# Optimization experiments

Hardware: AMD Instinct MI355X
Metric: run time of the kernel (lower is better)

## Reference

```python
import jax, jax.numpy as jnp
import numpy as np

L, D, F, V = 24, 1024, 4096, 50277  # n_layer, n_embd, ffn hidden (4*D), vocab
RESCALE = 6


def _ln(x, w, b, eps=1e-5):
    m = jnp.mean(x, axis=-1, keepdims=True)
    v = jnp.mean(jnp.square(x - m), axis=-1, keepdims=True)
    return (x - m) * jax.lax.rsqrt(v + eps) * w + b


def setup_inputs() -> dict:
    key = jax.random.key(0)
    ks = iter(jax.random.split(key, 64))

    def nrm(shape, s=0.02):
        return jax.random.normal(next(ks), shape, jnp.float32) * s

    def uni(shape):
        return jax.random.uniform(next(ks), shape, jnp.float32)

    state = jnp.zeros((L, 5, D), jnp.float32).at[:, 4, :].set(-1e30)  # pp init
    return {
        "token_embd": jax.random.normal(next(ks), (D,), jnp.float32),
        "state": state,
        "emb_ln_w": jnp.ones((D,), jnp.float32),
        "emb_ln_b": jnp.zeros((D,), jnp.float32),
        "ln1_w": jnp.ones((L, D), jnp.float32),
        "ln1_b": jnp.zeros((L, D), jnp.float32),
        "ln2_w": jnp.ones((L, D), jnp.float32),
        "ln2_b": jnp.zeros((L, D), jnp.float32),
        "att_tmk": uni((L, D)),
        "att_tmv": uni((L, D)),
        "att_tmr": uni((L, D)),
        "att_tf": nrm((L, D), 0.5),
        "att_td": -jnp.exp(nrm((L, D), 0.5)),  # time_decay = -exp(w) at load
        "att_kw": nrm((L, D, D)),
        "att_vw": nrm((L, D, D)),
        "att_rw": nrm((L, D, D)),
        "att_ow": nrm((L, D, D)),
        "ffn_tmk": uni((L, D)),
        "ffn_tmr": uni((L, D)),
        "ffn_kw": nrm((L, F, D)),
        "ffn_vw": nrm((L, D, F)),
        "ffn_rw": nrm((L, D, D)),
        "out_ln_w": jnp.ones((D,), jnp.float32),
        "out_ln_b": jnp.zeros((D,), jnp.float32),
        "head_w": nrm((V, D)),
    }


def reference(token_embd, state, emb_ln_w, emb_ln_b, ln1_w, ln1_b, ln2_w, ln2_b,
              att_tmk, att_tmv, att_tmr, att_tf, att_td, att_kw, att_vw, att_rw,
              att_ow, ffn_tmk, ffn_tmr, ffn_kw, ffn_vw, ffn_rw,
              out_ln_w, out_ln_b, head_w):
    x0 = _ln(token_embd, emb_ln_w, emb_ln_b)  # encoder

    def layer(x, inputs):
        (i, st, l1w, l1b, l2w, l2b, tmk, tmv, tmr, tf, td,
         kw, vw, rw, ow, ftmk, ftmr, fkw, fvw, frw) = inputs
        # ---- time mixing ----
        xn = _ln(x, l1w, l1b)
        s_att, aa, bb, pp = st[1], st[2], st[3], st[4]
        xk = xn * tmk + s_att * (1 - tmk)
        xv = xn * tmv + s_att * (1 - tmv)
        xr = xn * tmr + s_att * (1 - tmr)
        r = jax.nn.sigmoid(rw @ xr)
        kk = kw @ xk
        vv = vw @ xv
        ww = tf + kk
        p = jnp.maximum(pp, ww)
        e1 = jnp.exp(pp - p)
        e2 = jnp.exp(ww - p)
        a = e1 * aa + e2 * vv
        b = e1 * bb + e2
        ww2 = pp + td
        p2 = jnp.maximum(ww2, kk)
        f1 = jnp.exp(ww2 - p2)
        f2 = jnp.exp(kk - p2)
        new_aa = f1 * aa + f2 * vv
        new_bb = f1 * bb + f2
        x = x + ow @ (r * (a / b))
        # ---- channel mixing ----
        xn2 = _ln(x, l2w, l2b)
        s_ffn = st[0]
        xk2 = xn2 * ftmk + s_ffn * (1 - ftmk)
        xr2 = xn2 * ftmr + s_ffn * (1 - ftmr)
        r2 = jax.nn.sigmoid(frw @ xr2)
        k2 = jnp.square(jax.nn.relu(fkw @ xk2))
        x = x + r2 * (fvw @ k2)
        # rescale every RESCALE layers
        x = jnp.where((i + 1) % RESCALE == 0, x * 0.5, x)
        new_st = jnp.stack([xn2, xn, new_aa, new_bb, p2])
        return x, new_st

    idx = jnp.arange(L)
    x, new_state = jax.lax.scan(
        layer, x0,
        (idx, state, ln1_w, ln1_b, ln2_w, ln2_b, att_tmk, att_tmv, att_tmr,
         att_tf, att_td, att_kw, att_vw, att_rw, att_ow, ffn_tmk, ffn_tmr,
         ffn_kw, ffn_vw, ffn_rw))
    logits = head_w @ _ln(x, out_ln_w, out_ln_b)  # decoder
    return logits, new_state
```

## Files before the change

kernel.cpp:

```cpp
#include <hip/hip_runtime.h>

#define DD 1024
#define FF 4096
#define LL 24
#define VV 50277

typedef float v4f __attribute__((ext_vector_type(4)));


__device__ __forceinline__ float wave_sum(float v) {
#pragma unroll
    for (int o = 32; o > 0; o >>= 1) v += __shfl_xor(v, o, 64);
    return v;
}

__device__ __forceinline__ v4f ln_fast(v4f x, const float* __restrict__ w,
                                       const float* __restrict__ b,
                                       float* scr, int t) {
    float s1 = x[0] + x[1] + x[2] + x[3];
    float s2 = x[0]*x[0] + x[1]*x[1] + x[2]*x[2] + x[3]*x[3];
    s1 = wave_sum(s1); s2 = wave_sum(s2);
    int wv = t >> 6;
    __syncthreads();
    if ((t & 63) == 0) { scr[wv] = s1; scr[4 + wv] = s2; }
    __syncthreads();
    float S1 = scr[0] + scr[1] + scr[2] + scr[3];
    float S2 = scr[4] + scr[5] + scr[6] + scr[7];
    float m = S1 * (1.0f / 1024.0f);
    float var = S2 * (1.0f / 1024.0f) - m * m;
    float rs = rsqrtf(var + 1e-5f);
    v4f w4 = ((const v4f*)w)[t], b4 = ((const v4f*)b)[t];
    return (x - m) * rs * w4 + b4;
}

__device__ __forceinline__ v4f mixv(v4f n, v4f s, v4f m) { return n * m + s * (1.0f - m); }

__device__ __forceinline__ float dotv(v4f a, v4f x) {
    return fmaf(a[0], x[0], fmaf(a[1], x[1], fmaf(a[2], x[2], a[3] * x[3])));
}

struct Row { v4f a, b, c, d; };

__device__ __forceinline__ void row_load(Row& r, const float* p, int lane) {
    const v4f* q = (const v4f*)p;
    r.a = q[lane]; r.b = q[lane + 64]; r.c = q[lane + 128]; r.d = q[lane + 192];
}
__device__ __forceinline__ void row_pin(Row& r) {
    asm volatile("" : "+v"(r.a), "+v"(r.b), "+v"(r.c), "+v"(r.d));
}
__device__ __forceinline__ float row_dot(const Row& r, const v4f* v, int lane) {
    return dotv(r.a, v[lane]) + dotv(r.b, v[lane + 64]) +
           dotv(r.c, v[lane + 128]) + dotv(r.d, v[lane + 192]);
}


__global__ __launch_bounds__(256) void k1_timemix(
    const float* __restrict__ xin, const float* __restrict__ st,
    const float* __restrict__ enc_w, const float* __restrict__ enc_b,
    const float* __restrict__ l1w, const float* __restrict__ l1b,
    const float* __restrict__ tmk, const float* __restrict__ tmv,
    const float* __restrict__ tmr,
    const float* __restrict__ kw, const float* __restrict__ vw,
    const float* __restrict__ rw,
    float* __restrict__ kk, float* __restrict__ vv, float* __restrict__ rr,
    float* __restrict__ x0out, float* __restrict__ st_out) {
    __shared__ __align__(16) v4f s_k[256], s_v[256], s_r[256];
    __shared__ float scr[8];
    const int t = threadIdx.x, lane = t & 63, w = t >> 6, b = blockIdx.x;

    const int ridx = 4 * b + w, m = ridx >> 10, row = ridx & 1023;
    Row W;
    row_load(W, (m == 0 ? kw : m == 1 ? vw : rw) + (size_t)row * DD, lane);
    row_pin(W);

    v4f xv = ((const v4f*)xin)[t];
    if (enc_w) xv = ln_fast(xv, enc_w, enc_b, scr, t);
    if (x0out && b == 0) ((v4f*)x0out)[t] = xv;
    v4f n = ln_fast(xv, l1w, l1b, scr, t);
    if (b == 0) ((v4f*)(st_out + DD))[t] = n;
    {
        v4f sa = ((const v4f*)(st + DD))[t];
        s_k[t] = mixv(n, sa, ((const v4f*)tmk)[t]);
        s_v[t] = mixv(n, sa, ((const v4f*)tmv)[t]);
        s_r[t] = mixv(n, sa, ((const v4f*)tmr)[t]);
    }
    __syncthreads();

    const v4f* vec = (m == 0) ? s_k : (m == 1) ? s_v : s_r;
    float acc = wave_sum(row_dot(W, vec, lane));
    if (lane == 0) {
        if (m == 0)      kk[row] = acc;
        else if (m == 1) vv[row] = acc;
        else             rr[row] = 1.0f / (1.0f + expf(-acc));
    }
}


__global__ __launch_bounds__(256) void k2_wkv_out(
    const float* __restrict__ st, const float* __restrict__ tf,
    const float* __restrict__ td,
    const float* __restrict__ kk, const float* __restrict__ vv,
    const float* __restrict__ rr, const float* __restrict__ ow,
    float* __restrict__ x, float* __restrict__ st_out) {
    __shared__ __align__(16) v4f rab[256];
    const int t = threadIdx.x, lane = t & 63, w = t >> 6, b = blockIdx.x;

    const int row = 4 * b + w;
    Row W;
    row_load(W, ow + (size_t)row * DD, lane);
    row_pin(W);

    {
        v4f kx = ((const v4f*)kk)[t];
        v4f vx = ((const v4f*)vv)[t];
        v4f rx = ((const v4f*)rr)[t];
        v4f aa = ((const v4f*)(st + 2 * DD))[t];
        v4f bb = ((const v4f*)(st + 3 * DD))[t];
        v4f pp = ((const v4f*)(st + 4 * DD))[t];
        v4f tf4 = ((const v4f*)tf)[t];
        v4f td4 = ((const v4f*)td)[t];
        v4f rb, naa, nbb, np2;
#pragma unroll
        for (int c = 0; c < 4; ++c) {
            float kc = kx[c], vc = vx[c];
            float wwc = tf4[c] + kc;
            float p = fmaxf(pp[c], wwc);
            float e1 = expf(pp[c] - p), e2 = expf(wwc - p);
            rb[c] = rx[c] * ((e1 * aa[c] + e2 * vc) / (e1 * bb[c] + e2));
            float ww2 = pp[c] + td4[c];
            float p2 = fmaxf(ww2, kc);
            float f1 = expf(ww2 - p2), f2 = expf(kc - p2);
            naa[c] = f1 * aa[c] + f2 * vc;
            nbb[c] = f1 * bb[c] + f2;
            np2[c] = p2;
        }
        rab[t] = rb;
        if (b == 0) {
            ((v4f*)(st_out + 2 * DD))[t] = naa;
            ((v4f*)(st_out + 3 * DD))[t] = nbb;
            ((v4f*)(st_out + 4 * DD))[t] = np2;
        }
    }
    __syncthreads();

    float acc = wave_sum(row_dot(W, &rab[0], lane));
    if (lane == 0) x[row] += acc;
}


__global__ __launch_bounds__(256) void k3_ffn_kr(
    const float* __restrict__ x, const float* __restrict__ st,
    const float* __restrict__ l2w, const float* __restrict__ l2b,
    const float* __restrict__ ftmk, const float* __restrict__ ftmr,
    const float* __restrict__ fkw, const float* __restrict__ frw,
    float* __restrict__ k2, float* __restrict__ r2, float* __restrict__ st_out) {
    __shared__ __align__(16) v4f s_k[256], s_r[256];
    __shared__ float scr[8];
    const int t = threadIdx.x, lane = t & 63, w = t >> 6, b = blockIdx.x;

    const int ridx = 4 * b + w;
    Row W;
    row_load(W, (ridx < FF ? fkw + (size_t)ridx * DD
                           : frw + (size_t)(ridx - FF) * DD), lane);
    row_pin(W);

    v4f xv = ((const v4f*)x)[t];
    v4f n = ln_fast(xv, l2w, l2b, scr, t);
    if (b == 0) ((v4f*)st_out)[t] = n;
    {
        v4f sf = ((const v4f*)st)[t];
        s_k[t] = mixv(n, sf, ((const v4f*)ftmk)[t]);
        s_r[t] = mixv(n, sf, ((const v4f*)ftmr)[t]);
    }
    __syncthreads();

    const v4f* vec = (ridx < FF) ? s_k : s_r;
    float acc = wave_sum(row_dot(W, vec, lane));
    if (lane == 0) {
        if (ridx < FF) { float rl = fmaxf(acc, 0.f); k2[ridx] = rl * rl; }
        else           r2[ridx - FF] = 1.0f / (1.0f + expf(-acc));
    }
}


__global__ __launch_bounds__(256) void k4_ffn_v(
    const float* __restrict__ fvw, const float* __restrict__ k2,
    const float* __restrict__ r2, float* __restrict__ x, float scale) {
    __shared__ __align__(16) v4f k2s[1024];
    const int t = threadIdx.x, lane = t & 63, w = t >> 6, b = blockIdx.x;
    const int row = 4 * b + w;
    const v4f* W4 = (const v4f*)(fvw + (size_t)row * FF);

    v4f h0 = W4[lane],       h1 = W4[lane + 64],  h2 = W4[lane + 128], h3 = W4[lane + 192];
    v4f h4 = W4[lane + 256], h5 = W4[lane + 320], h6 = W4[lane + 384], h7 = W4[lane + 448];
    asm volatile("" : "+v"(h0), "+v"(h1), "+v"(h2), "+v"(h3),
                      "+v"(h4), "+v"(h5), "+v"(h6), "+v"(h7));

#pragma unroll
    for (int j = 0; j < 4; ++j)
        k2s[t + 256 * j] = ((const v4f*)k2)[t + 256 * j];
    __syncthreads();

    float acc = dotv(h0, k2s[lane])       + dotv(h1, k2s[lane + 64]) +
                dotv(h2, k2s[lane + 128]) + dotv(h3, k2s[lane + 192]) +
                dotv(h4, k2s[lane + 256]) + dotv(h5, k2s[lane + 320]) +
                dotv(h6, k2s[lane + 384]) + dotv(h7, k2s[lane + 448]);
#pragma unroll
    for (int j = 8; j < 16; ++j) {
        v4f a = W4[lane + 64 * j];
        acc += dotv(a, k2s[lane + 64 * j]);
    }
    acc = wave_sum(acc);
    if (lane == 0) x[row] = (x[row] + r2[row] * acc) * scale;
}


__global__ __launch_bounds__(256) void k_head(const float* __restrict__ head_w,
                                              const float* __restrict__ x,
                                              const float* __restrict__ olw,
                                              const float* __restrict__ olb,
                                              float* __restrict__ logits) {
    __shared__ __align__(16) v4f xs[256];
    __shared__ float scr[8];
    const int t = threadIdx.x, lane = t & 63, w = t >> 6;
    const int row = blockIdx.x * 4 + w;
    Row W;
    if (row < VV) { row_load(W, head_w + (size_t)row * DD, lane); row_pin(W); }

    v4f xv = ((const v4f*)x)[t];
    v4f nx = ln_fast(xv, olw, olb, scr, t);
    xs[t] = nx;
    __syncthreads();
    if (row < VV) {
        float acc = wave_sum(row_dot(W, &xs[0], lane));
        if (lane == 0) logits[row] = acc;
    }
}


extern "C" void kernel_launch(void* const* d_in, const int* in_sizes, int n_in,
                              void* d_out, int out_size, void* d_ws, size_t ws_size,
                              hipStream_t stream) {
    const float* token_embd = (const float*)d_in[0];
    const float* state      = (const float*)d_in[1];
    const float* emb_ln_w   = (const float*)d_in[2];
    const float* emb_ln_b   = (const float*)d_in[3];
    const float* ln1_w      = (const float*)d_in[4];
    const float* ln1_b      = (const float*)d_in[5];
    const float* ln2_w      = (const float*)d_in[6];
    const float* ln2_b      = (const float*)d_in[7];
    const float* att_tmk    = (const float*)d_in[8];
    const float* att_tmv    = (const float*)d_in[9];
    const float* att_tmr    = (const float*)d_in[10];
    const float* att_tf     = (const float*)d_in[11];
    const float* att_td     = (const float*)d_in[12];
    const float* att_kw     = (const float*)d_in[13];
    const float* att_vw     = (const float*)d_in[14];
    const float* att_rw     = (const float*)d_in[15];
    const float* att_ow     = (const float*)d_in[16];
    const float* ffn_tmk    = (const float*)d_in[17];
    const float* ffn_tmr    = (const float*)d_in[18];
    const float* ffn_kw     = (const float*)d_in[19];
    const float* ffn_vw     = (const float*)d_in[20];
    const float* ffn_rw     = (const float*)d_in[21];
    const float* out_ln_w   = (const float*)d_in[22];
    const float* out_ln_b   = (const float*)d_in[23];
    const float* head_w     = (const float*)d_in[24];

    float* logits = (float*)d_out;
    float* st_out_base = (float*)d_out + VV;

    float* ws  = (float*)d_ws;
    float* x   = ws;
    float* kk  = ws + 1024;
    float* vv  = ws + 2048;
    float* rr  = ws + 3072;
    float* k2b = ws + 4096;
    float* r2b = ws + 8192;

    for (int i = 0; i < LL; ++i) {
        const float* st = state + (size_t)i * 5 * DD;
        float* sto = st_out_base + (size_t)i * 5 * DD;

        k1_timemix<<<768, 256, 0, stream>>>(
            (i == 0) ? token_embd : x, st,
            (i == 0) ? emb_ln_w : nullptr, (i == 0) ? emb_ln_b : nullptr,
            ln1_w + i * DD, ln1_b + i * DD,
            att_tmk + i * DD, att_tmv + i * DD, att_tmr + i * DD,
            att_kw + (size_t)i * DD * DD, att_vw + (size_t)i * DD * DD,
            att_rw + (size_t)i * DD * DD,
            kk, vv, rr, (i == 0) ? x : nullptr, sto);

        k2_wkv_out<<<256, 256, 0, stream>>>(
            st, att_tf + i * DD, att_td + i * DD, kk, vv, rr,
            att_ow + (size_t)i * DD * DD, x, sto);

        k3_ffn_kr<<<1280, 256, 0, stream>>>(
            x, st, ln2_w + i * DD, ln2_b + i * DD,
            ffn_tmk + i * DD, ffn_tmr + i * DD,
            ffn_kw + (size_t)i * FF * DD, ffn_rw + (size_t)i * DD * DD,
            k2b, r2b, sto);

        float scale = ((i + 1) % 6 == 0) ? 0.5f : 1.0f;
        k4_ffn_v<<<256, 256, 0, stream>>>(
            ffn_vw + (size_t)i * DD * FF, k2b, r2b, x, scale);
    }

    k_head<<<(VV + 3) / 4, 256, 0, stream>>>(head_w, x, out_ln_w, out_ln_b, logits);
}
```

Baseline: 595.8 us.

## Fuse WKV into time-mix kernel and split output GEMVs across more blocks

The time-mix kernel now launches 768-thread blocks, each computing the k, v and r rows for the same 4 channels. That lets it evaluate the WKV recurrence and state update in-block and write r*wkv directly. The separate WKV pass is removed, and the att_ow and ffn_vw GEMVs are re-split so each block handles one output row across 4 waves (1024 blocks instead of 256). The aim is to raise parallelism and memory-level concurrency on bandwidth-bound matvecs and to drop one intermediate round-trip. In exchange it adds extra block-level reductions, and the LayerNorm in k1 runs with 12 waves, 8 of them idle.

```diff
diff --git a/kernel.cpp b/kernel.cpp
--- a/kernel.cpp
+++ b/kernel.cpp
@@ -14,22 +14,25 @@
     return v;
 }
 
-__device__ __forceinline__ v4f ln_fast(v4f x, const float* __restrict__ w,
-                                       const float* __restrict__ b,
-                                       float* scr, int t) {
-    float s1 = x[0] + x[1] + x[2] + x[3];
-    float s2 = x[0]*x[0] + x[1]*x[1] + x[2]*x[2] + x[3]*x[3];
+template <int NW>
+__device__ __forceinline__ v4f ln_gen(v4f x, const float* __restrict__ w,
+                                      const float* __restrict__ b,
+                                      float* scr, int t, bool act) {
+    float s1 = act ? (x[0] + x[1] + x[2] + x[3]) : 0.f;
+    float s2 = act ? (x[0]*x[0] + x[1]*x[1] + x[2]*x[2] + x[3]*x[3]) : 0.f;
     s1 = wave_sum(s1); s2 = wave_sum(s2);
     int wv = t >> 6;
     __syncthreads();
-    if ((t & 63) == 0) { scr[wv] = s1; scr[4 + wv] = s2; }
-    __syncthreads();
-    float S1 = scr[0] + scr[1] + scr[2] + scr[3];
-    float S2 = scr[4] + scr[5] + scr[6] + scr[7];
+    if ((t & 63) == 0) { scr[wv] = s1; scr[NW + wv] = s2; }
+    __syncthreads();
+    float S1 = 0.f, S2 = 0.f;
+#pragma unroll
+    for (int i = 0; i < NW; ++i) { S1 += scr[i]; S2 += scr[NW + i]; }
     float m = S1 * (1.0f / 1024.0f);
     float var = S2 * (1.0f / 1024.0f) - m * m;
     float rs = rsqrtf(var + 1e-5f);
-    v4f w4 = ((const v4f*)w)[t], b4 = ((const v4f*)b)[t];
+    v4f w4 = act ? ((const v4f*)w)[t] : (v4f){0.f, 0.f, 0.f, 0.f};
+    v4f b4 = act ? ((const v4f*)b)[t] : (v4f){0.f, 0.f, 0.f, 0.f};
     return (x - m) * rs * w4 + b4;
 }
 
@@ -54,97 +57,83 @@
 }
 
 
-__global__ __launch_bounds__(256) void k1_timemix(
+__global__ __launch_bounds__(768) void k1_timemix(
     const float* __restrict__ xin, const float* __restrict__ st,
     const float* __restrict__ enc_w, const float* __restrict__ enc_b,
     const float* __restrict__ l1w, const float* __restrict__ l1b,
     const float* __restrict__ tmk, const float* __restrict__ tmv,
-    const float* __restrict__ tmr,
+    const float* __restrict__ tmr, const float* __restrict__ tf,
+    const float* __restrict__ td,
     const float* __restrict__ kw, const float* __restrict__ vw,
     const float* __restrict__ rw,
-    float* __restrict__ kk, float* __restrict__ vv, float* __restrict__ rr,
-    float* __restrict__ x0out, float* __restrict__ st_out) {
-    __shared__ __align__(16) v4f s_k[256], s_v[256], s_r[256];
-    __shared__ float scr[8];
+    float* __restrict__ rab, float* __restrict__ x0out, float* __restrict__ sto) {
+    __shared__ __align__(16) v4f s_mix[3][256];
+    __shared__ float kvrL[3][4];
+    __shared__ float scr[24];
     const int t = threadIdx.x, lane = t & 63, w = t >> 6, b = blockIdx.x;
 
-    const int ridx = 4 * b + w, m = ridx >> 10, row = ridx & 1023;
-    Row W;
-    row_load(W, (m == 0 ? kw : m == 1 ? vw : rw) + (size_t)row * DD, lane);
-    row_pin(W);
-
-    v4f xv = ((const v4f*)xin)[t];
-    if (enc_w) xv = ln_fast(xv, enc_w, enc_b, scr, t);
-    if (x0out && b == 0) ((v4f*)x0out)[t] = xv;
-    v4f n = ln_fast(xv, l1w, l1b, scr, t);
-    if (b == 0) ((v4f*)(st_out + DD))[t] = n;
+    const int m = w >> 2, ch4 = w & 3;
+    Row R;
+    row_load(R, (m == 0 ? kw : m == 1 ? vw : rw) + (size_t)(4 * b + ch4) * DD, lane);
+    row_pin(R);
+
+    v4f xv = {0.f, 0.f, 0.f, 0.f};
+    if (t < 256) xv = ((const v4f*)xin)[t];
+    if (enc_w) xv = ln_gen<12>(xv, enc_w, enc_b, scr, t, t < 256);
+    if (x0out && b == 0 && t < 256) ((v4f*)x0out)[t] = xv;
+    v4f n = ln_gen<12>(xv, l1w, l1b, scr, t, t < 256);
+    if (t < 256) {
+        if (b == 0) ((v4f*)(sto + DD))[t] = n;
+        v4f sa = ((const v4f*)(st + DD))[t];
+        s_mix[0][t] = mixv(n, sa, ((const v4f*)tmk)[t]);
+        s_mix[1][t] = mixv(n, sa, ((const v4f*)tmv)[t]);
+        s_mix[2][t] = mixv(n, sa, ((const v4f*)tmr)[t]);
+    }
+    __syncthreads();
+
     {
-        v4f sa = ((const v4f*)(st + DD))[t];
-        s_k[t] = mixv(n, sa, ((const v4f*)tmk)[t]);
-        s_v[t] = mixv(n, sa, ((const v4f*)tmv)[t]);
-        s_r[t] = mixv(n, sa, ((const v4f*)tmr)[t]);
-    }
-    __syncthreads();
-
-    const v4f* vec = (m == 0) ? s_k : (m == 1) ? s_v : s_r;
-    float acc = wave_sum(row_dot(W, vec, lane));
-    if (lane == 0) {
-        if (m == 0)      kk[row] = acc;
-        else if (m == 1) vv[row] = acc;
-        else             rr[row] = 1.0f / (1.0f + expf(-acc));
-    }
-}
-
-
-__global__ __launch_bounds__(256) void k2_wkv_out(
-    const float* __restrict__ st, const float* __restrict__ tf,
-    const float* __restrict__ td,
-    const float* __restrict__ kk, const float* __restrict__ vv,
-    const float* __restrict__ rr, const float* __restrict__ ow,
-    float* __restrict__ x, float* __restrict__ st_out) {
-    __shared__ __align__(16) v4f rab[256];
-    const int t = threadIdx.x, lane = t & 63, w = t >> 6, b = blockIdx.x;
-
-    const int row = 4 * b + w;
-    Row W;
-    row_load(W, ow + (size_t)row * DD, lane);
-    row_pin(W);
-
-    {
-        v4f kx = ((const v4f*)kk)[t];
-        v4f vx = ((const v4f*)vv)[t];
-        v4f rx = ((const v4f*)rr)[t];
-        v4f aa = ((const v4f*)(st + 2 * DD))[t];
-        v4f bb = ((const v4f*)(st + 3 * DD))[t];
-        v4f pp = ((const v4f*)(st + 4 * DD))[t];
-        v4f tf4 = ((const v4f*)tf)[t];
-        v4f td4 = ((const v4f*)td)[t];
-        v4f rb, naa, nbb, np2;
-#pragma unroll
-        for (int c = 0; c < 4; ++c) {
-            float kc = kx[c], vc = vx[c];
-            float wwc = tf4[c] + kc;
-            float p = fmaxf(pp[c], wwc);
-            float e1 = expf(pp[c] - p), e2 = expf(wwc - p);
-            rb[c] = rx[c] * ((e1 * aa[c] + e2 * vc) / (e1 * bb[c] + e2));
-            float ww2 = pp[c] + td4[c];
-            float p2 = fmaxf(ww2, kc);
-            float f1 = expf(ww2 - p2), f2 = expf(kc - p2);
-            naa[c] = f1 * aa[c] + f2 * vc;
-            nbb[c] = f1 * bb[c] + f2;
-            np2[c] = p2;
-        }
-        rab[t] = rb;
-        if (b == 0) {
-            ((v4f*)(st_out + 2 * DD))[t] = naa;
-            ((v4f*)(st_out + 3 * DD))[t] = nbb;
-            ((v4f*)(st_out + 4 * DD))[t] = np2;
-        }
-    }
-    __syncthreads();
-
-    float acc = wave_sum(row_dot(W, &rab[0], lane));
-    if (lane == 0) x[row] += acc;
+        float acc = wave_sum(row_dot(R, &s_mix[m][0], lane));
+        if (lane == 0) kvrL[m][ch4] = acc;
+    }
+    __syncthreads();
+
+    if (t < 4) {
+        const int c = 4 * b + t;
+        float kk = kvrL[0][t], vv = kvrL[1][t];
+        float rr = 1.0f / (1.0f + expf(-kvrL[2][t]));
+        float aa = st[2 * DD + c], bb = st[3 * DD + c], pp = st[4 * DD + c];
+        float ww = tf[c] + kk;
+        float p = fmaxf(pp, ww);
+        float e1 = expf(pp - p), e2 = expf(ww - p);
+        rab[c] = rr * ((e1 * aa + e2 * vv) / (e1 * bb + e2));
+        float ww2 = pp + td[c];
+        float p2 = fmaxf(ww2, kk);
+        float f1 = expf(ww2 - p2), f2 = expf(kk - p2);
+        sto[2 * DD + c] = f1 * aa + f2 * vv;
+        sto[3 * DD + c] = f1 * bb + f2;
+        sto[4 * DD + c] = p2;
+    }
+}
+
+
+__global__ __launch_bounds__(256) void k2_ow(
+    const float* __restrict__ ow, const float* __restrict__ rab,
+    float* __restrict__ x) {
+    __shared__ __align__(16) v4f s_rab[256];
+    __shared__ float s_part[4];
+    const int t = threadIdx.x, lane = t & 63, w = t >> 6, r = blockIdx.x;
+
+    v4f wv = *(const v4f*)(ow + (size_t)r * DD + 4 * t);
+    asm volatile("" : "+v"(wv));
+
+    s_rab[t] = ((const v4f*)rab)[t];
+    __syncthreads();
+
+    float acc = wave_sum(dotv(wv, s_rab[w * 64 + lane]));
+    if (lane == 0) s_part[w] = acc;
+    __syncthreads();
+    if (t == 0)
+        x[r] += s_part[0] + s_part[1] + s_part[2] + s_part[3];
 }
 
 
@@ -165,7 +154,7 @@
     row_pin(W);
 
     v4f xv = ((const v4f*)x)[t];
-    v4f n = ln_fast(xv, l2w, l2b, scr, t);
+    v4f n = ln_gen<4>(xv, l2w, l2b, scr, t, true);
     if (b == 0) ((v4f*)st_out)[t] = n;
     {
         v4f sf = ((const v4f*)st)[t];
@@ -174,7 +163,7 @@
     }
     __syncthreads();
 
-    const v4f* vec = (ridx < FF) ? s_k : s_r;
+    const v4f* vec = (ridx < FF) ? &s_k[0] : &s_r[0];
     float acc = wave_sum(row_dot(W, vec, lane));
     if (lane == 0) {
         if (ridx < FF) { float rl = fmaxf(acc, 0.f); k2[ridx] = rl * rl; }
@@ -187,31 +176,28 @@
     const float* __restrict__ fvw, const float* __restrict__ k2,
     const float* __restrict__ r2, float* __restrict__ x, float scale) {
     __shared__ __align__(16) v4f k2s[1024];
-    const int t = threadIdx.x, lane = t & 63, w = t >> 6, b = blockIdx.x;
-    const int row = 4 * b + w;
-    const v4f* W4 = (const v4f*)(fvw + (size_t)row * FF);
-
-    v4f h0 = W4[lane],       h1 = W4[lane + 64],  h2 = W4[lane + 128], h3 = W4[lane + 192];
-    v4f h4 = W4[lane + 256], h5 = W4[lane + 320], h6 = W4[lane + 384], h7 = W4[lane + 448];
-    asm volatile("" : "+v"(h0), "+v"(h1), "+v"(h2), "+v"(h3),
-                      "+v"(h4), "+v"(h5), "+v"(h6), "+v"(h7));
+    __shared__ float s_part[4];
+    const int t = threadIdx.x, lane = t & 63, w = t >> 6, r = blockIdx.x;
+
+    const v4f* W4 = (const v4f*)(fvw + (size_t)r * FF) + (size_t)w * 256;
+    v4f w0 = W4[lane], w1 = W4[lane + 64], w2 = W4[lane + 128], w3 = W4[lane + 192];
+    asm volatile("" : "+v"(w0), "+v"(w1), "+v"(w2), "+v"(w3));
 
 #pragma unroll
     for (int j = 0; j < 4; ++j)
         k2s[t + 256 * j] = ((const v4f*)k2)[t + 256 * j];
     __syncthreads();
 
-    float acc = dotv(h0, k2s[lane])       + dotv(h1, k2s[lane + 64]) +
-                dotv(h2, k2s[lane + 128]) + dotv(h3, k2s[lane + 192]) +
-                dotv(h4, k2s[lane + 256]) + dotv(h5, k2s[lane + 320]) +
-                dotv(h6, k2s[lane + 384]) + dotv(h7, k2s[lane + 448]);
-#pragma unroll
-    for (int j = 8; j < 16; ++j) {
-        v4f a = W4[lane + 64 * j];
-        acc += dotv(a, k2s[lane + 64 * j]);
-    }
+    const v4f* kq = &k2s[w * 256];
+    float acc = dotv(w0, kq[lane]) + dotv(w1, kq[lane + 64]) +
+                dotv(w2, kq[lane + 128]) + dotv(w3, kq[lane + 192]);
     acc = wave_sum(acc);
-    if (lane == 0) x[row] = (x[row] + r2[row] * acc) * scale;
+    if (lane == 0) s_part[w] = acc;
+    __syncthreads();
+    if (t == 0) {
+        float sum = s_part[0] + s_part[1] + s_part[2] + s_part[3];
+        x[r] = (x[r] + r2[r] * sum) * scale;
+    }
 }
 
 
@@ -228,7 +214,7 @@
     if (row < VV) { row_load(W, head_w + (size_t)row * DD, lane); row_pin(W); }
 
     v4f xv = ((const v4f*)x)[t];
-    v4f nx = ln_fast(xv, olw, olb, scr, t);
+    v4f nx = ln_gen<4>(xv, olw, olb, scr, t, true);
     xs[t] = nx;
     __syncthreads();
     if (row < VV) {
@@ -270,30 +256,28 @@
     float* logits = (float*)d_out;
     float* st_out_base = (float*)d_out + VV;
 
-    float* ws  = (float*)d_ws;
-    float* x   = ws;
-    float* kk  = ws + 1024;
-    float* vv  = ws + 2048;
-    float* rr  = ws + 3072;
-    float* k2b = ws + 4096;
-    float* r2b = ws + 8192;
+    float* ws   = (float*)d_ws;
+    float* x    = ws;
+    float* rab  = ws + 1024;
+    float* k2b  = ws + 2048;
+    float* r2b  = ws + 6144;
 
     for (int i = 0; i < LL; ++i) {
         const float* st = state + (size_t)i * 5 * DD;
         float* sto = st_out_base + (size_t)i * 5 * DD;
 
-        k1_timemix<<<768, 256, 0, stream>>>(
+        k1_timemix<<<256, 768, 0, stream>>>(
             (i == 0) ? token_embd : x, st,
             (i == 0) ? emb_ln_w : nullptr, (i == 0) ? emb_ln_b : nullptr,
             ln1_w + i * DD, ln1_b + i * DD,
             att_tmk + i * DD, att_tmv + i * DD, att_tmr + i * DD,
+            att_tf + i * DD, att_td + i * DD,
             att_kw + (size_t)i * DD * DD, att_vw + (size_t)i * DD * DD,
             att_rw + (size_t)i * DD * DD,
-            kk, vv, rr, (i == 0) ? x : nullptr, sto);
-
-        k2_wkv_out<<<256, 256, 0, stream>>>(
-            st, att_tf + i * DD, att_td + i * DD, kk, vv, rr,
-            att_ow + (size_t)i * DD * DD, x, sto);
+            rab, (i == 0) ? x : nullptr, sto);
+
+        k2_ow<<<1024, 256, 0, stream>>>(
+            att_ow + (size_t)i * DD * DD, rab, x);
 
         k3_ffn_kr<<<1280, 256, 0, stream>>>(
             x, st, ln2_w + i * DD, ln2_b + i * DD,
@@ -302,7 +286,7 @@
             k2b, r2b, sto);
 
         float scale = ((i + 1) % 6 == 0) ? 0.5f : 1.0f;
-        k4_ffn_v<<<256, 256, 0, stream>>>(
+        k4_ffn_v<<<1024, 256, 0, stream>>>(
             ffn_vw + (size_t)i * DD * FF, k2b, r2b, x, scale);
     }
 
```

New measurement: 582.9 us. 1.02x faster.
